# Performance work log

Hardware: AMD Instinct MI355X
Metric: run time of the kernel (lower is better)

## Reference

```python
import jax, jax.numpy as jnp
import numpy as np

BETA = 0.2
ALPHA_NEG = 0.8
ALPHA_POS = 0.2
EPS = 1e-8  # torch cosine_similarity eps

B, D, P = 8192, 256, 4096


def setup_inputs() -> dict:
    key = jax.random.key(0)
    k1, k2 = jax.random.split(key)
    embeddings = jax.random.normal(k1, (B, D), dtype=jnp.float32)
    positive_pairs = jax.random.randint(k2, (P, 2), 0, B, dtype=jnp.int32)
    return {"embeddings": embeddings, "positive_pairs": positive_pairs}


def reference(embeddings, positive_pairs):
    b = embeddings.shape[0]
    p = positive_pairs.shape[0]
    # cosine similarity matrix (normalize once, single GEMM)
    nrm = jnp.maximum(jnp.linalg.norm(embeddings, axis=1, keepdims=True), EPS)
    e = embeddings / nrm
    cos = e @ e.T                              # [B, B]
    exp_cos = jnp.exp(cos / BETA)
    ii = positive_pairs[:, 0]
    jj = positive_pairs[:, 1]
    # mask = eye + positive pairs (both directions)
    mask = jnp.eye(b, dtype=bool)
    mask = mask.at[ii, jj].set(True).at[jj, ii].set(True)
    exp_masked = jnp.where(mask, 0.0, exp_cos)  # masked_fill(mask, 0)
    pos_ij = exp_cos[ii, jj]                   # [P]
    pos_ji = exp_cos[jj, ii]                   # [P]
    exp_i = exp_masked[ii]                     # [P, B]
    exp_j = exp_masked[jj]                     # [P, B]
    # hard-negative mining via alpha_neg quantile per row
    thr_i = jnp.quantile(exp_i, ALPHA_NEG, axis=1, keepdims=True)
    thr_j = jnp.quantile(exp_j, ALPHA_NEG, axis=1, keepdims=True)
    S_i = jnp.sum(jnp.where(exp_i >= thr_i, exp_i, 0.0), axis=1)  # [P]
    S_j = jnp.sum(jnp.where(exp_j >= thr_j, exp_j, 0.0), axis=1)  # [P]
    # hard-positive mining via alpha_pos quantile
    thr_pij = jnp.quantile(pos_ij, ALPHA_POS)
    thr_pji = jnp.quantile(pos_ji, ALPHA_POS)
    sel_ij = pos_ij <= thr_pij
    sel_ji = pos_ji <= thr_pji
    # torch loop zips the two (order-preserving) boolean-selected lists ->
    # truncates to min count; values are never cross-coupled, only the count.
    kmin = jnp.minimum(sel_ij.sum(), sel_ji.sum())
    act_ij = sel_ij & ((jnp.cumsum(sel_ij.astype(jnp.int32)) - 1) < kmin)
    act_ji = sel_ji & ((jnp.cumsum(sel_ji.astype(jnp.int32)) - 1) < kmin)
    # -log(pk / (pk + S[m])) = log1p(S[m] / pk), summed over all m per pk
    term_ij = jnp.log1p(S_i[None, :] / pos_ij[:, None])  # [P, P]
    term_ji = jnp.log1p(S_j[None, :] / pos_ji[:, None])  # [P, P]
    loss = (jnp.sum(term_ij * act_ij[:, None].astype(term_ij.dtype))
            + jnp.sum(term_ji * act_ji[:, None].astype(term_ji.dtype)))
    return loss / (2.0 * p)
```

## Files before the change

### kernel.cpp

```cpp
#include <hip/hip_runtime.h>
#include <stdint.h>

#define BN    8192
#define DK    256
#define PN    4096
#define MAXP  16
#define QSTEP 0.02f
#define WLO   134
#define KEEP  1639u
#define SPLITS 8
#define CPS   1024
#define NPART 64
#define PWORDS 12

typedef float f32x4  __attribute__((ext_vector_type(4)));
typedef int   i32x4  __attribute__((ext_vector_type(4)));

#define MF(a,b,c) __builtin_amdgcn_mfma_i32_16x16x64_i8(a, b, c, 0, 0, 0)

__device__ __forceinline__ void find_bin_256(const unsigned* hist, int rank,
                                             int* sh, unsigned* wtot) {
  const int tid = threadIdx.x, lane = tid & 63, w = tid >> 6;
  unsigned x = hist[tid];
  unsigned pref = x;
  #pragma unroll
  for (int o = 1; o < 64; o <<= 1) {
    unsigned y = __shfl_up(pref, o);
    if (lane >= o) pref += y;
  }
  if (lane == 63) wtot[w] = pref;
  __syncthreads();
  unsigned woff = 0;
  for (int i = 0; i < w; ++i) woff += wtot[i];
  unsigned incl = pref + woff, excl = incl - x;
  if ((unsigned)rank >= excl && (unsigned)rank < incl) { sh[0] = tid; sh[1] = rank - (int)excl; }
  __syncthreads();
}

__device__ __forceinline__ float block_sum4(float x, float* red4) {
  const int lane = threadIdx.x & 63, w = threadIdx.x >> 6;
  #pragma unroll
  for (int o = 32; o; o >>= 1) x += __shfl_xor(x, o);
  __syncthreads();
  if (lane == 0) red4[w] = x;
  __syncthreads();
  return red4[0] + red4[1] + red4[2] + red4[3];
}

__global__ void __launch_bounds__(256) norm_pairs_kernel(
    const float* __restrict__ X, signed char* __restrict__ Ei8,
    const int2* __restrict__ pairs, int* pcount, int* partners,
    int* rowlist, int* cnt) {
  const int tid  = threadIdx.x;
  const int lane = tid & 63;
  const int wib  = tid >> 6;
  const int row  = blockIdx.x * 4 + wib;

  float4 x = ((const float4*)(X + (size_t)row * DK))[lane];
  float ss = x.x * x.x + x.y * x.y + x.z * x.z + x.w * x.w;
  #pragma unroll
  for (int o = 32; o; o >>= 1) ss += __shfl_xor(ss, o);
  float inv = 127.0f / fmaxf(sqrtf(ss), 1e-8f);
  int c0 = (int)rintf(inv * x.x);
  int c1 = (int)rintf(inv * x.y);
  int c2 = (int)rintf(inv * x.z);
  int c3 = (int)rintf(inv * x.w);
  unsigned u = (unsigned)(c0 & 255) | ((unsigned)(c1 & 255) << 8)
             | ((unsigned)(c2 & 255) << 16) | ((unsigned)(c3 & 255) << 24);
  ((unsigned*)(Ei8 + (size_t)row * DK))[lane] = u;

  const int p = blockIdx.x * 256 + tid;
  if (p < PN) {
    int2 pr = pairs[p];
    int ix = atomicAdd(&pcount[pr.x], 1);
    if (ix == 0) { int q = atomicAdd(cnt, 1); rowlist[q] = pr.x; }
    if (ix < MAXP) partners[pr.x * MAXP + ix] = pr.y;
    int iy = atomicAdd(&pcount[pr.y], 1);
    if (iy == 0) { int q = atomicAdd(cnt, 1); rowlist[q] = pr.y; }
    if (iy < MAXP) partners[pr.y * MAXP + iy] = pr.x;
  }
}

__global__ void __launch_bounds__(256) pos_kernel(
    const signed char* __restrict__ Ei8, const int2* __restrict__ pairs,
    float* __restrict__ pos) {
  const int tid  = threadIdx.x;
  const int lane = tid & 63;
  const int wib  = tid >> 6;
  const int p    = blockIdx.x * 4 + wib;
  int2 pr = pairs[p];
  int a = ((const int*)(Ei8 + (size_t)pr.x * DK))[lane];
  int b = ((const int*)(Ei8 + (size_t)pr.y * DK))[lane];
  int s = 0;
  #pragma unroll
  for (int j = 0; j < 4; ++j) {
    int va = (int)(signed char)(a >> (8 * j));
    int vb = (int)(signed char)(b >> (8 * j));
    s += va * vb;
  }
  #pragma unroll
  for (int o = 32; o; o >>= 1) s += __shfl_xor(s, o);
  if (lane == 0) pos[p] = __expf((float)s * (5.0f / 16129.0f));
}

#define UPD(A, V) do {                                              \
    int code_ = (int)fmaf((float)(V), SCL, 128.5f);                 \
    if (code_ > 255) code_ = 255;                                   \
    int idx_ = code_ - WLO;                                         \
    unsigned one_ = ((unsigned)idx_ < 16u) ? (1u << ((idx_ & 3) << 3)) : 0u; \
    int wd_ = idx_ >> 2;                                            \
    wc##A##0 += (wd_ == 0) ? one_ : 0u;                             \
    wc##A##1 += (wd_ == 1) ? one_ : 0u;                             \
    wc##A##2 += (wd_ == 2) ? one_ : 0u;                             \
    wc##A##3 += (wd_ == 3) ? one_ : 0u;                             \
    unsigned hi_ = (code_ >= WLO + 16) ? 1u : 0u;                   \
    chi##A += hi_;                                                  \
    float v_ = __expf((float)(code_ - 128) * QSTEP);                \
    sx##A += hi_ ? v_ : 0.f;                                        \
  } while (0)

#define ROWDECL(A) unsigned wc##A##0=0,wc##A##1=0,wc##A##2=0,wc##A##3=0,chi##A=0; float sx##A=0.f;

#define ROWSTORE(A, AIDX) do {                                      \
    const int row_ = rbase + ((AIDX) >> 2) * 16 + q * 4 + ((AIDX) & 3); \
    unsigned p0 = wc##A##0 & 0xFF00FFu, p1 = (wc##A##0 >> 8) & 0xFF00FFu; \
    unsigned p2 = wc##A##1 & 0xFF00FFu, p3 = (wc##A##1 >> 8) & 0xFF00FFu; \
    unsigned p4 = wc##A##2 & 0xFF00FFu, p5 = (wc##A##2 >> 8) & 0xFF00FFu; \
    unsigned p6 = wc##A##3 & 0xFF00FFu, p7 = (wc##A##3 >> 8) & 0xFF00FFu; \
    unsigned ch = chi##A; float s_ = sx##A;                         \
    _Pragma("unroll")                                               \
    for (int o = 1; o < 16; o <<= 1) {                              \
      p0 += __shfl_xor(p0, o); p1 += __shfl_xor(p1, o);             \
      p2 += __shfl_xor(p2, o); p3 += __shfl_xor(p3, o);             \
      p4 += __shfl_xor(p4, o); p5 += __shfl_xor(p5, o);             \
      p6 += __shfl_xor(p6, o); p7 += __shfl_xor(p7, o);             \
      ch += __shfl_xor(ch, o); s_ += __shfl_xor(s_, o);             \
    }                                                               \
    if (cl == 0) {                                                  \
      unsigned* dst = part + ((size_t)row_ * NPART + sp) * PWORDS;  \
      dst[0]=p0; dst[1]=p1; dst[2]=p2; dst[3]=p3; dst[4]=p4;        \
      dst[5]=p5; dst[6]=p6; dst[7]=p7; dst[8]=ch;                   \
      ((float*)dst)[9]=s_;                                          \
    }                                                               \
  } while (0)

__global__ void __launch_bounds__(512) gemm_stats_kernel(
    const signed char* __restrict__ Ei8, const int* __restrict__ rowlist,
    const int* __restrict__ countp, unsigned* __restrict__ part) {
  const int cnt = *countp;
  const int rbase = blockIdx.y * 32;
  if (rbase >= cnt) return;
  const int tid = threadIdx.x, lane = tid & 63, w = tid >> 6;
  const int q  = lane >> 4;
  const int cl = lane & 15;

  i32x4 afr[2][4];
  #pragma unroll
  for (int g = 0; g < 2; ++g) {
    int rr = rbase + g * 16 + cl;
    int grow = (rr < cnt) ? rowlist[rr] : 0;
    const signed char* ap = Ei8 + (size_t)grow * DK + q * 16;
    #pragma unroll
    for (int kb = 0; kb < 4; ++kb)
      afr[g][kb] = *(const i32x4*)(ap + kb * 64);
  }

  ROWDECL(0) ROWDECL(1) ROWDECL(2) ROWDECL(3)
  ROWDECL(4) ROWDECL(5) ROWDECL(6) ROWDECL(7)

  const float SCL = 250.0f / 16129.0f;
  const int colbase = blockIdx.x * CPS + w * 16 + cl;

  i32x4 b0, b1, b2, b3, n0, n1, n2, n3;
  {
    const signed char* bp = Ei8 + (size_t)colbase * DK + q * 16;
    b0 = *(const i32x4*)(bp);
    b1 = *(const i32x4*)(bp + 64);
    b2 = *(const i32x4*)(bp + 128);
    b3 = *(const i32x4*)(bp + 192);
  }
  for (int c = 0; c < CPS / 128; ++c) {
    if (c < CPS / 128 - 1) {
      const signed char* bp = Ei8 + (size_t)(colbase + (c + 1) * 128) * DK + q * 16;
      n0 = *(const i32x4*)(bp);
      n1 = *(const i32x4*)(bp + 64);
      n2 = *(const i32x4*)(bp + 128);
      n3 = *(const i32x4*)(bp + 192);
    }
    i32x4 acc0 = {0, 0, 0, 0}, acc1 = {0, 0, 0, 0};
    acc0 = MF(afr[0][0], b0, acc0); acc1 = MF(afr[1][0], b0, acc1);
    acc0 = MF(afr[0][1], b1, acc0); acc1 = MF(afr[1][1], b1, acc1);
    acc0 = MF(afr[0][2], b2, acc0); acc1 = MF(afr[1][2], b2, acc1);
    acc0 = MF(afr[0][3], b3, acc0); acc1 = MF(afr[1][3], b3, acc1);
    UPD(0, acc0[0]); UPD(1, acc0[1]); UPD(2, acc0[2]); UPD(3, acc0[3]);
    UPD(4, acc1[0]); UPD(5, acc1[1]); UPD(6, acc1[2]); UPD(7, acc1[3]);
    b0 = n0; b1 = n1; b2 = n2; b3 = n3;
  }

  const int sp = blockIdx.x * 8 + w;
  ROWSTORE(0, 0); ROWSTORE(1, 1); ROWSTORE(2, 2); ROWSTORE(3, 3);
  ROWSTORE(4, 4); ROWSTORE(5, 5); ROWSTORE(6, 6); ROWSTORE(7, 7);
}

__global__ void __launch_bounds__(256) row_stats_kernel(
    const unsigned* __restrict__ part, const signed char* __restrict__ Ei8,
    const int* __restrict__ rowlist, const int* __restrict__ countp,
    const int* __restrict__ pcount, const int* __restrict__ partners,
    float* __restrict__ S) {
  const int cnt = *countp;
  const int g = blockIdx.x;
  if (g * 4 >= cnt) return;
  __shared__ int plist[4][MAXP + 1];
  __shared__ int npl[4];
  __shared__ int growl[4];
  const int tid = threadIdx.x, lane = tid & 63, w = tid >> 6;

  if (tid < 4) {
    int rr = g * 4 + tid;
    int grow = (rr < cnt) ? rowlist[rr] : -1;
    growl[tid] = grow;
    int np = 0;
    if (grow >= 0) {
      np = pcount[grow]; if (np > MAXP) np = MAXP;
      for (int e = 0; e < np; ++e) plist[tid][e] = partners[grow * MAXP + e];
      plist[tid][np] = grow; np++;
    }
    npl[tid] = np;
  }
  __syncthreads();

  const int rr = g * 4 + w;
  const int grow = growl[w];
  if (grow < 0) return;

  const unsigned* src = part + ((size_t)rr * NPART + lane) * PWORDS;
  uint4 A = *(const uint4*)src;
  uint4 B = *(const uint4*)(src + 4);
  unsigned ch = src[8];
  float sxf = ((const float*)src)[9];
  #pragma unroll
  for (int o = 1; o < 64; o <<= 1) {
    A.x += __shfl_xor(A.x, o); A.y += __shfl_xor(A.y, o);
    A.z += __shfl_xor(A.z, o); A.w += __shfl_xor(A.w, o);
    B.x += __shfl_xor(B.x, o); B.y += __shfl_xor(B.y, o);
    B.z += __shfl_xor(B.z, o); B.w += __shfl_xor(B.w, o);
    ch  += __shfl_xor(ch, o);  sxf += __shfl_xor(sxf, o);
  }

  const int arow = ((const int*)(Ei8 + (size_t)grow * DK))[lane];
  const int np = npl[w];
  for (int e = 0; e < np; ++e) {
    const int col = plist[w][e];
    bool dup = false;
    for (int f = 0; f < e; ++f) if (plist[w][f] == col) { dup = true; break; }
    if (dup) continue;
    const int bcol = ((const int*)(Ei8 + (size_t)col * DK))[lane];
    int s = 0;
    #pragma unroll
    for (int j = 0; j < 4; ++j) {
      int va = (int)(signed char)(arow >> (8 * j));
      int vb = (int)(signed char)(bcol >> (8 * j));
      s += va * vb;
    }
    #pragma unroll
    for (int o = 32; o; o >>= 1) s += __shfl_xor(s, o);
    int code = (int)fmaf((float)s, 250.0f / 16129.0f, 128.5f);
    if (code > 255) code = 255;
    if (code >= WLO + 16) {
      ch -= 1u;
      sxf -= __expf((float)(code - 128) * QSTEP);
    } else if (code >= WLO) {
      int idx = code - WLO;
      unsigned dec = 1u << (((idx >> 1) & 1) * 16);
      int wd = 2 * (idx >> 2) + (idx & 1);
      A.x -= (wd == 0) ? dec : 0u; A.y -= (wd == 1) ? dec : 0u;
      A.z -= (wd == 2) ? dec : 0u; A.w -= (wd == 3) ? dec : 0u;
      B.x -= (wd == 4) ? dec : 0u; B.y -= (wd == 5) ? dec : 0u;
      B.z -= (wd == 6) ? dec : 0u; B.w -= (wd == 7) ? dec : 0u;
    }
  }

  unsigned cbin = 0;
  {
    int wd = 2 * (lane >> 2) + (lane & 1);
    unsigned wsel = (wd == 0) ? A.x : (wd == 1) ? A.y : (wd == 2) ? A.z :
                    (wd == 3) ? A.w : (wd == 4) ? B.x : (wd == 5) ? B.y :
                    (wd == 6) ? B.z : B.w;
    cbin = ((lane >> 1) & 1) ? (wsel >> 16) : (wsel & 0xFFFFu);
    if (lane >= 16) cbin = 0;
  }
  unsigned pref = cbin;
  #pragma unroll
  for (int o = 1; o < 16; o <<= 1) {
    unsigned y = __shfl_up(pref, o);
    if (lane >= o) pref += y;
  }
  const unsigned total16 = __shfl(pref, 15);
  const unsigned suffix = total16 - pref;
  const unsigned Cb = ch + suffix;
  bool isb = (lane < 16) && (Cb < KEEP) && (Cb + cbin >= KEEP);
  unsigned long long m = __ballot(isb);
  float Sval = sxf;
  if (m != 0ULL) {
    const int bsel = __ffsll(m) - 1;
    const unsigned need = KEEP - __shfl(Cb, bsel);
    const float val = __expf((float)(WLO + lane - 128) * QSTEP);
    float contrib = 0.f;
    if (lane < 16) {
      if (lane > bsel)       contrib = (float)cbin * val;
      else if (lane == bsel) contrib = (float)need * val;
    }
    #pragma unroll
    for (int o = 32; o; o >>= 1) contrib += __shfl_xor(contrib, o);
    Sval += contrib;
  }
  if (lane == 0) S[grow] = Sval;
}

__global__ void __launch_bounds__(256) finale_kernel(
    const float* __restrict__ pos, const int2* __restrict__ pairs,
    const float* __restrict__ S, float* __restrict__ out) {
  __shared__ uint32_t v[PN];
  __shared__ unsigned hist[256];
  __shared__ int sh[2];
  __shared__ unsigned wtot[4];
  __shared__ float red4[4];
  const int tid = threadIdx.x;
  for (int i = tid; i < PN; i += 256) v[i] = ((const uint32_t*)pos)[i];
  __syncthreads();
  int rank = 819;
  uint32_t prefix = 0;
  for (int pass = 0; pass < 4; ++pass) {
    const int shift = 24 - pass * 8;
    hist[tid] = 0;
    __syncthreads();
    for (int i = tid; i < PN; i += 256) {
      uint32_t x = v[i];
      bool match = (pass == 0) || ((x >> (shift + 8)) == (prefix >> (shift + 8)));
      if (match) atomicAdd(&hist[(x >> shift) & 255u], 1u);
    }
    __syncthreads();
    find_bin_256(hist, rank, sh, wtot);
    prefix |= ((uint32_t)sh[0]) << shift;
    rank = sh[1];
    __syncthreads();
  }
  float thr; __builtin_memcpy(&thr, &prefix, 4);

  float n = 0.f, sl = 0.f, sp = 0.f, sp2 = 0.f;
  for (int r = tid; r < PN; r += 256) {
    float p; uint32_t b = v[r]; __builtin_memcpy(&p, &b, 4);
    if (p <= thr) { n += 1.f; sl += __logf(p); sp += p; sp2 += p * p; }
  }
  float t = 0.f, u = 0.f, vv = 0.f;
  for (int c = tid; c < PN; c += 256) {
    int2 pr = pairs[c];
    float s1 = S[pr.x], s2 = S[pr.y];
    float i1 = 1.f / s1, i2 = 1.f / s2;
    t += __logf(s1) + __logf(s2);
    u += i1 + i2;
    vv += i1 * i1 + i2 * i2;
  }
  const float N   = block_sum4(n, red4);
  const float SL  = block_sum4(sl, red4);
  const float SP  = block_sum4(sp, red4);
  const float SP2 = block_sum4(sp2, red4);
  const float T   = block_sum4(t, red4);
  const float U   = block_sum4(u, red4);
  const float V   = block_sum4(vv, red4);
  if (tid == 0) {
    double num = (double)N * T - 2.0 * (double)PN * (double)SL
               + (double)SP * U - 0.5 * (double)SP2 * V;
    out[0] = (float)(num / (2.0 * (double)PN));
  }
}

extern "C" void kernel_launch(void* const* d_in, const int* in_sizes, int n_in,
                              void* d_out, int out_size, void* d_ws, size_t ws_size,
                              hipStream_t stream) {
  const float* emb  = (const float*)d_in[0];
  const int2* pairs = (const int2*)d_in[1];
  float* out = (float*)d_out;

  char* w = (char*)d_ws;
  size_t off = 0;
  int*         pcnt  = (int*)(w + off);         off += (size_t)BN * 4;
  int*         rlist = (int*)(w + off);         off += (size_t)BN * 4;
  int*         cnt   = (int*)(w + off);         off += 256;
  signed char* Ei8   = (signed char*)(w + off); off += (size_t)BN * DK;
  float*       S     = (float*)(w + off);       off += (size_t)BN * 4;
  float*       pos   = (float*)(w + off);       off += (size_t)PN * 4;
  int*         parts = (int*)(w + off);         off += (size_t)BN * MAXP * 4;
  unsigned*    part  = (unsigned*)(w + off);    off += (size_t)BN * NPART * PWORDS * 4;

  hipMemsetAsync(pcnt, 0, (size_t)BN * 8 + 256, stream);
  norm_pairs_kernel<<<BN / 4, 256, 0, stream>>>(emb, Ei8, pairs, pcnt, parts, rlist, cnt);
  pos_kernel<<<PN / 4, 256, 0, stream>>>(Ei8, pairs, pos);
  gemm_stats_kernel<<<dim3(SPLITS, BN / 32), 512, 0, stream>>>(Ei8, rlist, cnt, part);
  row_stats_kernel<<<BN / 4, 256, 0, stream>>>(part, Ei8, rlist, cnt, pcnt, parts, S);
  finale_kernel<<<1, 256, 0, stream>>>(pos, pairs, S, out);
}
```

Before: 182.0 us.

## Pack histogram into 64-bit nibble counters and streamline per-element stats update

Replaces four 32-bit byte-packed bin counters per row with a single 64-bit word of 4-bit counters and computes the bin directly from the integer dot product, which cuts register use and ALU work in the inner loop. The exp now uses the raw dot product instead of a quantized code, which changes numerics slightly. The loop is manually unrolled with ping-pong B buffers instead of copying registers, and launch bounds request 4 waves per SIMD. Nibble counters can overflow if more than 15 hits land in one bin per lane over 8 chunks; the maximum per lane is exactly 8, so this is safe here.

```diff
diff --git a/kernel.cpp b/kernel.cpp
--- a/kernel.cpp
+++ b/kernel.cpp
@@ -12,6 +12,8 @@
 #define CPS   1024
 #define NPART 64
 #define PWORDS 12
+#define SCLF (250.0f / 16129.0f)
+#define K1E  (5.0f / 16129.0f)
 
 typedef float f32x4  __attribute__((ext_vector_type(4)));
 typedef int   i32x4  __attribute__((ext_vector_type(4)));
@@ -100,51 +102,71 @@
   }
   #pragma unroll
   for (int o = 32; o; o >>= 1) s += __shfl_xor(s, o);
-  if (lane == 0) pos[p] = __expf((float)s * (5.0f / 16129.0f));
-}
-
-#define UPD(A, V) do {                                              \
-    int code_ = (int)fmaf((float)(V), SCL, 128.5f);                 \
-    if (code_ > 255) code_ = 255;                                   \
-    int idx_ = code_ - WLO;                                         \
-    unsigned one_ = ((unsigned)idx_ < 16u) ? (1u << ((idx_ & 3) << 3)) : 0u; \
-    int wd_ = idx_ >> 2;                                            \
-    wc##A##0 += (wd_ == 0) ? one_ : 0u;                             \
-    wc##A##1 += (wd_ == 1) ? one_ : 0u;                             \
-    wc##A##2 += (wd_ == 2) ? one_ : 0u;                             \
-    wc##A##3 += (wd_ == 3) ? one_ : 0u;                             \
-    unsigned hi_ = (code_ >= WLO + 16) ? 1u : 0u;                   \
-    chi##A += hi_;                                                  \
-    float v_ = __expf((float)(code_ - 128) * QSTEP);                \
-    sx##A += hi_ ? v_ : 0.f;                                        \
+  if (lane == 0) pos[p] = __expf((float)s * K1E);
+}
+
+#define UPD4(WC, CHI, SX, DOT) do {                                  \
+    int t_ = (DOT) - 355;                                            \
+    float df_ = (float)(DOT);                                        \
+    int bin_ = (int)fmaf(df_, SCLF, -5.5f);                          \
+    unsigned long long oh_ = 1ull << ((bin_ << 2) & 63);             \
+    WC += ((unsigned)t_ < 1033u) ? oh_ : 0ull;                       \
+    bool hi_ = (t_ >= 1033);                                         \
+    CHI += hi_ ? 1u : 0u;                                            \
+    float v_ = __expf(df_ * K1E);                                    \
+    SX += hi_ ? v_ : 0.f;                                            \
   } while (0)
 
-#define ROWDECL(A) unsigned wc##A##0=0,wc##A##1=0,wc##A##2=0,wc##A##3=0,chi##A=0; float sx##A=0.f;
-
-#define ROWSTORE(A, AIDX) do {                                      \
+#define ROWDECL(A) unsigned long long wc##A = 0ull; unsigned chi##A = 0u; float sx##A = 0.f;
+
+#define ROWSTORE(A, AIDX) do {                                       \
     const int row_ = rbase + ((AIDX) >> 2) * 16 + q * 4 + ((AIDX) & 3); \
-    unsigned p0 = wc##A##0 & 0xFF00FFu, p1 = (wc##A##0 >> 8) & 0xFF00FFu; \
-    unsigned p2 = wc##A##1 & 0xFF00FFu, p3 = (wc##A##1 >> 8) & 0xFF00FFu; \
-    unsigned p4 = wc##A##2 & 0xFF00FFu, p5 = (wc##A##2 >> 8) & 0xFF00FFu; \
-    unsigned p6 = wc##A##3 & 0xFF00FFu, p7 = (wc##A##3 >> 8) & 0xFF00FFu; \
-    unsigned ch = chi##A; float s_ = sx##A;                         \
-    _Pragma("unroll")                                               \
-    for (int o = 1; o < 16; o <<= 1) {                              \
-      p0 += __shfl_xor(p0, o); p1 += __shfl_xor(p1, o);             \
-      p2 += __shfl_xor(p2, o); p3 += __shfl_xor(p3, o);             \
-      p4 += __shfl_xor(p4, o); p5 += __shfl_xor(p5, o);             \
-      p6 += __shfl_xor(p6, o); p7 += __shfl_xor(p7, o);             \
-      ch += __shfl_xor(ch, o); s_ += __shfl_xor(s_, o);             \
-    }                                                               \
-    if (cl == 0) {                                                  \
-      unsigned* dst = part + ((size_t)row_ * NPART + sp) * PWORDS;  \
-      dst[0]=p0; dst[1]=p1; dst[2]=p2; dst[3]=p3; dst[4]=p4;        \
-      dst[5]=p5; dst[6]=p6; dst[7]=p7; dst[8]=ch;                   \
-      ((float*)dst)[9]=s_;                                          \
-    }                                                               \
+    unsigned lo_ = (unsigned)wc##A, hi2_ = (unsigned)(wc##A >> 32);  \
+    unsigned p0 = (lo_ & 0xFu)         | (((lo_ >> 8)  & 0xFu) << 16); \
+    unsigned p1 = ((lo_ >> 4) & 0xFu)  | (((lo_ >> 12) & 0xFu) << 16); \
+    unsigned p2 = ((lo_ >> 16) & 0xFu) | (((lo_ >> 24) & 0xFu) << 16); \
+    unsigned p3 = ((lo_ >> 20) & 0xFu) | (((lo_ >> 28) & 0xFu) << 16); \
+    unsigned p4 = (hi2_ & 0xFu)         | (((hi2_ >> 8)  & 0xFu) << 16); \
+    unsigned p5 = ((hi2_ >> 4) & 0xFu)  | (((hi2_ >> 12) & 0xFu) << 16); \
+    unsigned p6 = ((hi2_ >> 16) & 0xFu) | (((hi2_ >> 24) & 0xFu) << 16); \
+    unsigned p7 = ((hi2_ >> 20) & 0xFu) | (((hi2_ >> 28) & 0xFu) << 16); \
+    unsigned ch = chi##A; float s_ = sx##A;                          \
+    _Pragma("unroll")                                                \
+    for (int o = 1; o < 16; o <<= 1) {                               \
+      p0 += __shfl_xor(p0, o); p1 += __shfl_xor(p1, o);              \
+      p2 += __shfl_xor(p2, o); p3 += __shfl_xor(p3, o);              \
+      p4 += __shfl_xor(p4, o); p5 += __shfl_xor(p5, o);              \
+      p6 += __shfl_xor(p6, o); p7 += __shfl_xor(p7, o);              \
+      ch += __shfl_xor(ch, o); s_ += __shfl_xor(s_, o);              \
+    }                                                                \
+    if (cl == 0) {                                                   \
+      unsigned* dst = part + ((size_t)row_ * NPART + sp) * PWORDS;   \
+      dst[0]=p0; dst[1]=p1; dst[2]=p2; dst[3]=p3; dst[4]=p4;         \
+      dst[5]=p5; dst[6]=p6; dst[7]=p7; dst[8]=ch;                    \
+      ((float*)dst)[9]=s_;                                           \
+    }                                                                \
   } while (0)
 
-__global__ void __launch_bounds__(512) gemm_stats_kernel(
+#define CHUNK(BX0,BX1,BX2,BX3, BY0,BY1,BY2,BY3, PC) do {             \
+    if ((PC) < CPS / 128) {                                          \
+      const signed char* bp_ = Ei8 + (size_t)(colbase + (PC) * 128) * DK + q * 16; \
+      BY0 = *(const i32x4*)(bp_);                                    \
+      BY1 = *(const i32x4*)(bp_ + 64);                               \
+      BY2 = *(const i32x4*)(bp_ + 128);                              \
+      BY3 = *(const i32x4*)(bp_ + 192);                              \
+    }                                                                \
+    i32x4 acc0 = {0,0,0,0}, acc1 = {0,0,0,0};                        \
+    acc0 = MF(afr[0][0], BX0, acc0); acc1 = MF(afr[1][0], BX0, acc1);\
+    acc0 = MF(afr[0][1], BX1, acc0); acc1 = MF(afr[1][1], BX1, acc1);\
+    acc0 = MF(afr[0][2], BX2, acc0); acc1 = MF(afr[1][2], BX2, acc1);\
+    acc0 = MF(afr[0][3], BX3, acc0); acc1 = MF(afr[1][3], BX3, acc1);\
+    UPD4(wc0, chi0, sx0, acc0[0]); UPD4(wc1, chi1, sx1, acc0[1]);    \
+    UPD4(wc2, chi2, sx2, acc0[2]); UPD4(wc3, chi3, sx3, acc0[3]);    \
+    UPD4(wc4, chi4, sx4, acc1[0]); UPD4(wc5, chi5, sx5, acc1[1]);    \
+    UPD4(wc6, chi6, sx6, acc1[2]); UPD4(wc7, chi7, sx7, acc1[3]);    \
+  } while (0)
+
+__global__ void __launch_bounds__(512, 4) gemm_stats_kernel(
     const signed char* __restrict__ Ei8, const int* __restrict__ rowlist,
     const int* __restrict__ countp, unsigned* __restrict__ part) {
   const int cnt = *countp;
@@ -168,34 +190,24 @@
   ROWDECL(0) ROWDECL(1) ROWDECL(2) ROWDECL(3)
   ROWDECL(4) ROWDECL(5) ROWDECL(6) ROWDECL(7)
 
-  const float SCL = 250.0f / 16129.0f;
   const int colbase = blockIdx.x * CPS + w * 16 + cl;
 
-  i32x4 b0, b1, b2, b3, n0, n1, n2, n3;
+  i32x4 bA0, bA1, bA2, bA3, bB0, bB1, bB2, bB3;
   {
     const signed char* bp = Ei8 + (size_t)colbase * DK + q * 16;
-    b0 = *(const i32x4*)(bp);
-    b1 = *(const i32x4*)(bp + 64);
-    b2 = *(const i32x4*)(bp + 128);
-    b3 = *(const i32x4*)(bp + 192);
-  }
-  for (int c = 0; c < CPS / 128; ++c) {
-    if (c < CPS / 128 - 1) {
-      const signed char* bp = Ei8 + (size_t)(colbase + (c + 1) * 128) * DK + q * 16;
-      n0 = *(const i32x4*)(bp);
-      n1 = *(const i32x4*)(bp + 64);
-      n2 = *(const i32x4*)(bp + 128);
-      n3 = *(const i32x4*)(bp + 192);
-    }
-    i32x4 acc0 = {0, 0, 0, 0}, acc1 = {0, 0, 0, 0};
-    acc0 = MF(afr[0][0], b0, acc0); acc1 = MF(afr[1][0], b0, acc1);
-    acc0 = MF(afr[0][1], b1, acc0); acc1 = MF(afr[1][1], b1, acc1);
-    acc0 = MF(afr[0][2], b2, acc0); acc1 = MF(afr[1][2], b2, acc1);
-    acc0 = MF(afr[0][3], b3, acc0); acc1 = MF(afr[1][3], b3, acc1);
-    UPD(0, acc0[0]); UPD(1, acc0[1]); UPD(2, acc0[2]); UPD(3, acc0[3]);
-    UPD(4, acc1[0]); UPD(5, acc1[1]); UPD(6, acc1[2]); UPD(7, acc1[3]);
-    b0 = n0; b1 = n1; b2 = n2; b3 = n3;
-  }
+    bA0 = *(const i32x4*)(bp);
+    bA1 = *(const i32x4*)(bp + 64);
+    bA2 = *(const i32x4*)(bp + 128);
+    bA3 = *(const i32x4*)(bp + 192);
+  }
+  CHUNK(bA0,bA1,bA2,bA3, bB0,bB1,bB2,bB3, 1);
+  CHUNK(bB0,bB1,bB2,bB3, bA0,bA1,bA2,bA3, 2);
+  CHUNK(bA0,bA1,bA2,bA3, bB0,bB1,bB2,bB3, 3);
+  CHUNK(bB0,bB1,bB2,bB3, bA0,bA1,bA2,bA3, 4);
+  CHUNK(bA0,bA1,bA2,bA3, bB0,bB1,bB2,bB3, 5);
+  CHUNK(bB0,bB1,bB2,bB3, bA0,bA1,bA2,bA3, 6);
+  CHUNK(bA0,bA1,bA2,bA3, bB0,bB1,bB2,bB3, 7);
+  CHUNK(bB0,bB1,bB2,bB3, bA0,bA1,bA2,bA3, 8);
 
   const int sp = blockIdx.x * 8 + w;
   ROWSTORE(0, 0); ROWSTORE(1, 1); ROWSTORE(2, 2); ROWSTORE(3, 3);
@@ -264,15 +276,14 @@
     }
     #pragma unroll
     for (int o = 32; o; o >>= 1) s += __shfl_xor(s, o);
-    int code = (int)fmaf((float)s, 250.0f / 16129.0f, 128.5f);
-    if (code > 255) code = 255;
-    if (code >= WLO + 16) {
+    const int t = s - 355;
+    if (t >= 1033) {
       ch -= 1u;
-      sxf -= __expf((float)(code - 128) * QSTEP);
-    } else if (code >= WLO) {
-      int idx = code - WLO;
-      unsigned dec = 1u << (((idx >> 1) & 1) * 16);
-      int wd = 2 * (idx >> 2) + (idx & 1);
+      sxf -= __expf((float)s * K1E);
+    } else if ((unsigned)t < 1033u) {
+      int bin = (int)fmaf((float)s, SCLF, -5.5f);
+      unsigned dec = 1u << (((bin >> 1) & 1) * 16);
+      int wd = 2 * (bin >> 2) + (bin & 1);
       A.x -= (wd == 0) ? dec : 0u; A.y -= (wd == 1) ? dec : 0u;
       A.z -= (wd == 2) ? dec : 0u; A.w -= (wd == 3) ? dec : 0u;
       B.x -= (wd == 4) ? dec : 0u; B.y -= (wd == 5) ? dec : 0u;
```

Measured after the change: 189.0 us. 3.8% more time.
